# Optimization experiments

Measured on AMD Instinct MI355X. Metric: run time of the kernel, lower is better.

## Reference

```python
import jax, jax.numpy as jnp
import numpy as np

N = 8192
F_IN = 256
F_OUT = 64
ALPHA = 0.2  # LeakyReLU negative slope
NEG_INF = -9e15


def setup_inputs() -> dict:
    key = jax.random.key(0)
    k1, k2, k3, k4 = jax.random.split(key, 4)
    h = jax.random.normal(k1, (N, F_IN), dtype=jnp.float32)
    adj = jax.random.randint(k2, (N, N), 0, 2, dtype=jnp.int32)
    W = jax.random.normal(k3, (F_IN, F_OUT), dtype=jnp.float32) * 0.1
    a = jax.random.normal(k4, (2 * F_OUT, 1), dtype=jnp.float32) * 0.1
    return {"h": h, "adj": adj, "W": W, "a": a}


def reference(h, adj, W, a):
    # Wh: [N, F_out]
    Wh = h @ W
    # e_ij = LeakyReLU(a1 . Wh_i + a2 . Wh_j); same math as the O(N^2*2F)
    # concat in the original, computed via two [N] gathers + broadcast add.
    f_src = Wh @ a[:F_OUT, 0]   # [N] contribution of node i (row)
    f_dst = Wh @ a[F_OUT:, 0]   # [N] contribution of node j (col)
    e = f_src[:, None] + f_dst[None, :]          # [N, N]
    e = jnp.where(e > 0, e, ALPHA * e)           # LeakyReLU
    # masked softmax over neighbors (dim=1)
    e = jnp.where(adj > 0, e, NEG_INF)
    attention = jax.nn.softmax(e, axis=1)        # [N, N]
    h_prime = attention @ Wh                     # [N, F_out]
    # concat=True -> ELU
    return jax.nn.elu(h_prime)
```

## Files before the change

### kernel.cpp

```cpp
#include <hip/hip_runtime.h>
#include <math.h>

#define N 8192
#define FIN 256
#define FOUT 64
#define ALPHA 0.2f
#define LOG2E 1.442695040888963f

#define JT 256
#define NTILE (N / JT)
#define ROWPITCH 512
#define OFF_B 0
#define OFF_A (64 * ROWPITCH)
#define BUFB (OFF_A + 16 * ROWPITCH)
#define SMEM_BYTES (2 * BUFB)

typedef float f32x4 __attribute__((ext_vector_type(4)));
typedef _Float16 f16x8 __attribute__((ext_vector_type(8)));

__device__ __forceinline__ unsigned pack_f16(float a, float b) {
    union { _Float16 h; unsigned short u; } ca, cb;
    ca.h = (_Float16)a; cb.h = (_Float16)b;
    return (unsigned)ca.u | ((unsigned)cb.u << 16);
}
__device__ __forceinline__ float wcalc(int av, float fsr, float g) {
    float e = fsr + g;
    float le = e > 0.f ? e : ALPHA * e;
    float r = __builtin_exp2f(fmaf(le, LOG2E, -4.0f));
    return av != 0 ? r : 0.f;
}

__global__ __launch_bounds__(256) void gat_prep(
    const float* __restrict__ h, const float* __restrict__ W,
    const float* __restrict__ a,
    float* __restrict__ fsrc, float* __restrict__ fdst,
    unsigned short* __restrict__ WhT)
{
    __shared__ float sWh[16][FOUT + 1];
    const int t = threadIdx.x;
    const int f = t & 63;
    const int wq = t >> 6;
    const int row0 = blockIdx.x * 16;
    const int rbase = row0 + wq * 4;

    float acc[4] = {0.f, 0.f, 0.f, 0.f};
    for (int k0 = 0; k0 < FIN; k0 += 4) {
        const float w0 = W[(k0 + 0) * FOUT + f];
        const float w1 = W[(k0 + 1) * FOUT + f];
        const float w2 = W[(k0 + 2) * FOUT + f];
        const float w3 = W[(k0 + 3) * FOUT + f];
#pragma unroll
        for (int rr = 0; rr < 4; ++rr) {
            const float4 hv = *reinterpret_cast<const float4*>(
                &h[(size_t)(rbase + rr) * FIN + k0]);
            acc[rr] = fmaf(hv.x, w0, acc[rr]);
            acc[rr] = fmaf(hv.y, w1, acc[rr]);
            acc[rr] = fmaf(hv.z, w2, acc[rr]);
            acc[rr] = fmaf(hv.w, w3, acc[rr]);
        }
    }
    const float as = a[f], ad = a[FOUT + f];
#pragma unroll
    for (int rr = 0; rr < 4; ++rr) {
        sWh[wq * 4 + rr][f] = acc[rr];
        float fs = acc[rr] * as, fd = acc[rr] * ad;
#pragma unroll
        for (int off = 1; off < 64; off <<= 1) {
            fs += __shfl_xor(fs, off, 64);
            fd += __shfl_xor(fd, off, 64);
        }
        if (f == 0) { fsrc[rbase + rr] = fs; fdst[rbase + rr] = fd; }
    }
    __syncthreads();
    const int ff = t >> 2;
    const int r4 = (t & 3) * 4;
    uint2 v;
    v.x = pack_f16(sWh[r4 + 0][ff], sWh[r4 + 1][ff]);
    v.y = pack_f16(sWh[r4 + 2][ff], sWh[r4 + 3][ff]);
    *reinterpret_cast<uint2*>(&WhT[(size_t)ff * N + row0 + r4]) = v;
}

struct Regs { int4 a0, a1; float4 g0, g1; int4 b0, b1, b2, b3; };

__global__ __launch_bounds__(512, 4) void gat_main(
    const int* __restrict__ adj,
    const unsigned short* __restrict__ WhT,
    const float* __restrict__ fsrc, const float* __restrict__ fdst,
    float* __restrict__ out)
{
    __shared__ __align__(16) char smem[SMEM_BYTES];

    const int t = threadIdx.x;
    const int l = t & 63;
    const int w = t >> 6;
    const int row0 = blockIdx.x * 16;

    const int srow = t >> 5;
    const int sc8 = (t & 31) * 8;
    const int bf = t >> 3;
    const int bg = t & 7;
    const float fsr = fsrc[row0 + srow];
    const size_t adjrow = (size_t)(row0 + srow) * N;
    const size_t bfrow = (size_t)bf * N;

    const int aswz = (srow & 7) << 4;
    const int bswz = (bf & 7) << 4;
    const int awo  = OFF_A + srow * ROWPITCH + (((t & 31) * 16) ^ aswz);
    const int bwo0 = OFF_B + bf * ROWPITCH + (((bg + 0) * 16) ^ bswz);
    const int bwo1 = OFF_B + bf * ROWPITCH + (((bg + 8) * 16) ^ bswz);
    const int bwo2 = OFF_B + bf * ROWPITCH + (((bg + 16) * 16) ^ bswz);
    const int bwo3 = OFF_B + bf * ROWPITCH + (((bg + 24) * 16) ^ bswz);

    const int ft = w & 3;
    const int p = w >> 2;
    const int r16 = l & 15;
    const int kg8 = (l >> 4) << 3;
    const int fswz = (r16 & 7) << 4;
    const int aro = OFF_A + r16 * ROWPITCH;
    const int bro = OFF_B + (ft * 16 + r16) * ROWPITCH;

    f32x4 acc = {0.f, 0.f, 0.f, 0.f};
    float zacc = 0.f;
    Regs RA, RB;

#define BAR                                                                    \
    {                                                                          \
        asm volatile("s_waitcnt lgkmcnt(0)" ::: "memory");                     \
        __builtin_amdgcn_s_barrier();                                          \
    }

#define LOADG(tile, S)                                                         \
    {                                                                          \
        const int j0_ = (tile) * JT;                                           \
        S.a0 = *reinterpret_cast<const int4*>(&adj[adjrow + j0_ + sc8]);       \
        S.a1 = *reinterpret_cast<const int4*>(&adj[adjrow + j0_ + sc8 + 4]);   \
        S.g0 = *reinterpret_cast<const float4*>(&fdst[j0_ + sc8]);             \
        S.g1 = *reinterpret_cast<const float4*>(&fdst[j0_ + sc8 + 4]);         \
        S.b0 = *reinterpret_cast<const int4*>(&WhT[bfrow + j0_ + (bg+0)*8]);   \
        S.b1 = *reinterpret_cast<const int4*>(&WhT[bfrow + j0_ + (bg+8)*8]);   \
        S.b2 = *reinterpret_cast<const int4*>(&WhT[bfrow + j0_ + (bg+16)*8]);  \
        S.b3 = *reinterpret_cast<const int4*>(&WhT[bfrow + j0_ + (bg+24)*8]);  \
    }

#define STAGE(S, BUF)                                                          \
    {                                                                          \
        char* bs_ = smem + (BUF) * BUFB;                                       \
        *reinterpret_cast<int4*>(bs_ + bwo0) = S.b0;                           \
        *reinterpret_cast<int4*>(bs_ + bwo1) = S.b1;                           \
        *reinterpret_cast<int4*>(bs_ + bwo2) = S.b2;                           \
        *reinterpret_cast<int4*>(bs_ + bwo3) = S.b3;                           \
        const float w0 = wcalc(S.a0.x, fsr, S.g0.x);                           \
        const float w1 = wcalc(S.a0.y, fsr, S.g0.y);                           \
        const float w2 = wcalc(S.a0.z, fsr, S.g0.z);                           \
        const float w3 = wcalc(S.a0.w, fsr, S.g0.w);                           \
        const float w4 = wcalc(S.a1.x, fsr, S.g1.x);                           \
        const float w5 = wcalc(S.a1.y, fsr, S.g1.y);                           \
        const float w6 = wcalc(S.a1.z, fsr, S.g1.z);                           \
        const float w7 = wcalc(S.a1.w, fsr, S.g1.w);                           \
        zacc += (w0 + w1) + (w2 + w3) + ((w4 + w5) + (w6 + w7));               \
        uint4 pk;                                                              \
        pk.x = pack_f16(w0, w1); pk.y = pack_f16(w2, w3);                      \
        pk.z = pack_f16(w4, w5); pk.w = pack_f16(w6, w7);                      \
        *reinterpret_cast<uint4*>(bs_ + awo) = pk;                             \
    }

#define MFMA_PHASE(BUF)                                                        \
    {                                                                          \
        const char* bb_ = smem + (BUF) * BUFB;                                 \
        __builtin_amdgcn_s_setprio(1);                                         \
        _Pragma("unroll")                                                      \
        for (int ks = 0; ks < 4; ++ks) {                                       \
            const int cb = (p * 128 + ks * 32 + kg8) * 2;                      \
            const f16x8 af = *reinterpret_cast<const f16x8*>(bb_ + aro + (cb ^ fswz)); \
            const f16x8 bv = *reinterpret_cast<const f16x8*>(bb_ + bro + (cb ^ fswz)); \
            acc = __builtin_amdgcn_mfma_f32_16x16x32_f16(af, bv, acc, 0, 0, 0);\
        }                                                                      \
        __builtin_amdgcn_s_setprio(0);                                         \
    }

    LOADG(0, RA);
    LOADG(1, RB);
    STAGE(RA, 0);
    LOADG(2, RA);
    BAR;

    for (int tt = 0; tt < NTILE; tt += 2) {
        if (tt + 1 < NTILE) STAGE(RB, 1);
        if (tt + 3 < NTILE) LOADG(tt + 3, RB);
        MFMA_PHASE(0);
        BAR;
        if (tt + 2 < NTILE) STAGE(RA, 0);
        if (tt + 4 < NTILE) LOADG(tt + 4, RA);
        if (tt + 1 < NTILE) MFMA_PHASE(1);
        BAR;
    }
#undef LOADG
#undef STAGE
#undef MFMA_PHASE
#undef BAR

    float* zb = reinterpret_cast<float*>(smem + 8192);
    {
        float z = zacc;
#pragma unroll
        for (int off = 1; off < 32; off <<= 1) z += __shfl_xor(z, off, 64);
        if ((l & 31) == 0) zb[srow] = z;
    }

    *reinterpret_cast<f32x4*>(smem + w * 1024 + l * 16) = acc;
    __syncthreads();
#pragma unroll
    for (int e0 = 0; e0 < 2; ++e0) {
        const int e = t + e0 * 512;
        const int rr = e >> 6, f2 = e & 63;
        const int ft2 = f2 >> 4, n = f2 & 15;
        const int ln = n | ((rr >> 2) << 4);
        const int rg = rr & 3;
        const float s =
            *reinterpret_cast<const float*>(smem + ft2 * 1024 + ln * 16 + rg * 4) +
            *reinterpret_cast<const float*>(smem + (ft2 + 4) * 1024 + ln * 16 + rg * 4);
        const float hp = s / zb[rr];
        out[(size_t)(row0 + rr) * FOUT + f2] = hp > 0.f ? hp : expm1f(hp);
    }
}

extern "C" void kernel_launch(void* const* d_in, const int* in_sizes, int n_in,
                              void* d_out, int out_size, void* d_ws, size_t ws_size,
                              hipStream_t stream) {
    const float* h   = (const float*)d_in[0];
    const int*   adj = (const int*)d_in[1];
    const float* W   = (const float*)d_in[2];
    const float* a   = (const float*)d_in[3];
    float* out = (float*)d_out;

    float* ws = (float*)d_ws;
    float* fsrc = ws;
    float* fdst = fsrc + N;
    unsigned short* WhT = (unsigned short*)(fdst + N);

    gat_prep<<<dim3(N / 16), dim3(256), 0, stream>>>(h, W, a, fsrc, fdst, WhT);
    gat_main<<<dim3(N / 16), dim3(512), 0, stream>>>(adj, WhT, fsrc, fdst, out);
}
```

Baseline: 92.75 us.

## Prepack Wh into MFMA fragment layout and load B operands directly to registers

The prep kernel now writes Wh in a pre-swizzled MFMA B-fragment layout. The main kernel therefore loads B operands straight from global memory into registers and no longer stages them through LDS. This cuts LDS traffic and LDS footprint, which allows the launch-bounds occupancy hint to rise from 4 to 6. The pipeline is reordered to single-buffer the adj/fdst registers, and the prep kernel uses 32-row blocks. The cost is that each wave issues more redundant global/L2 reads of B, since these are no longer shared via LDS across the waves of a block.

```diff
diff --git a/kernel.cpp b/kernel.cpp
--- a/kernel.cpp
+++ b/kernel.cpp
@@ -10,13 +10,13 @@
 #define JT 256
 #define NTILE (N / JT)
 #define ROWPITCH 512
-#define OFF_B 0
-#define OFF_A (64 * ROWPITCH)
-#define BUFB (OFF_A + 16 * ROWPITCH)
-#define SMEM_BYTES (2 * BUFB)
+#define ABUF (16 * ROWPITCH)
+#define SMEM_BYTES (2 * ABUF)
 
 typedef float f32x4 __attribute__((ext_vector_type(4)));
 typedef _Float16 f16x8 __attribute__((ext_vector_type(8)));
+
+union F16V { uint4 u; f16x8 h; };
 
 __device__ __forceinline__ unsigned pack_f16(float a, float b) {
     union { _Float16 h; unsigned short u; } ca, cb;
@@ -30,17 +30,17 @@
     return av != 0 ? r : 0.f;
 }
 
-__global__ __launch_bounds__(256) void gat_prep(
+__global__ __launch_bounds__(512) void gat_prep(
     const float* __restrict__ h, const float* __restrict__ W,
     const float* __restrict__ a,
     float* __restrict__ fsrc, float* __restrict__ fdst,
-    unsigned short* __restrict__ WhT)
+    uint4* __restrict__ Bp)
 {
-    __shared__ float sWh[16][FOUT + 1];
+    __shared__ float sWh[32][FOUT + 1];
     const int t = threadIdx.x;
     const int f = t & 63;
     const int wq = t >> 6;
-    const int row0 = blockIdx.x * 16;
+    const int row0 = blockIdx.x * 32;
     const int rbase = row0 + wq * 4;
 
     float acc[4] = {0.f, 0.f, 0.f, 0.f};
@@ -72,19 +72,27 @@
         if (f == 0) { fsrc[rbase + rr] = fs; fdst[rbase + rr] = fd; }
     }
     __syncthreads();
-    const int ff = t >> 2;
-    const int r4 = (t & 3) * 4;
-    uint2 v;
-    v.x = pack_f16(sWh[r4 + 0][ff], sWh[r4 + 1][ff]);
-    v.y = pack_f16(sWh[r4 + 2][ff], sWh[r4 + 3][ff]);
-    *reinterpret_cast<uint2*>(&WhT[(size_t)ff * N + row0 + r4]) = v;
-}
-
-struct Regs { int4 a0, a1; float4 g0, g1; int4 b0, b1, b2, b3; };
-
-__global__ __launch_bounds__(512, 4) void gat_main(
+    if (t < 256) {
+        const int ft = t >> 6;
+        const int l = t & 63;
+        const int li = l & 15, g = l >> 4;
+        float v[8];
+#pragma unroll
+        for (int e = 0; e < 8; ++e) v[e] = sWh[g * 8 + e][ft * 16 + li];
+        uint4 pk;
+        pk.x = pack_f16(v[0], v[1]);
+        pk.y = pack_f16(v[2], v[3]);
+        pk.z = pack_f16(v[4], v[5]);
+        pk.w = pack_f16(v[6], v[7]);
+        Bp[(size_t)(blockIdx.x * 4 + ft) * 64 + l] = pk;
+    }
+}
+
+struct AdjG { int4 a0, a1; float4 g0, g1; };
+
+__global__ __launch_bounds__(512, 6) void gat_main(
     const int* __restrict__ adj,
-    const unsigned short* __restrict__ WhT,
+    const uint4* __restrict__ Bp,
     const float* __restrict__ fsrc, const float* __restrict__ fdst,
     float* __restrict__ out)
 {
@@ -97,31 +105,22 @@
 
     const int srow = t >> 5;
     const int sc8 = (t & 31) * 8;
-    const int bf = t >> 3;
-    const int bg = t & 7;
     const float fsr = fsrc[row0 + srow];
     const size_t adjrow = (size_t)(row0 + srow) * N;
-    const size_t bfrow = (size_t)bf * N;
-
-    const int aswz = (srow & 7) << 4;
-    const int bswz = (bf & 7) << 4;
-    const int awo  = OFF_A + srow * ROWPITCH + (((t & 31) * 16) ^ aswz);
-    const int bwo0 = OFF_B + bf * ROWPITCH + (((bg + 0) * 16) ^ bswz);
-    const int bwo1 = OFF_B + bf * ROWPITCH + (((bg + 8) * 16) ^ bswz);
-    const int bwo2 = OFF_B + bf * ROWPITCH + (((bg + 16) * 16) ^ bswz);
-    const int bwo3 = OFF_B + bf * ROWPITCH + (((bg + 24) * 16) ^ bswz);
+    const int awo = srow * ROWPITCH + (((t & 31) * 16) ^ ((srow & 7) << 4));
 
     const int ft = w & 3;
     const int p = w >> 2;
     const int r16 = l & 15;
     const int kg8 = (l >> 4) << 3;
     const int fswz = (r16 & 7) << 4;
-    const int aro = OFF_A + r16 * ROWPITCH;
-    const int bro = OFF_B + (ft * 16 + r16) * ROWPITCH;
+    const int aro = r16 * ROWPITCH;
+    const uint4* Bq = Bp + (size_t)p * 1024 + ft * 64 + l;
 
     f32x4 acc = {0.f, 0.f, 0.f, 0.f};
     float zacc = 0.f;
-    Regs RA, RB;
+    AdjG AG;
+    uint4 BA0, BA1, BA2, BA3, BB0, BB1, BB2, BB3;
 
 #define BAR                                                                    \
     {                                                                          \
@@ -129,76 +128,88 @@
         __builtin_amdgcn_s_barrier();                                          \
     }
 
-#define LOADG(tile, S)                                                         \
+#define LOAD_ADJG(tile)                                                        \
     {                                                                          \
         const int j0_ = (tile) * JT;                                           \
-        S.a0 = *reinterpret_cast<const int4*>(&adj[adjrow + j0_ + sc8]);       \
-        S.a1 = *reinterpret_cast<const int4*>(&adj[adjrow + j0_ + sc8 + 4]);   \
-        S.g0 = *reinterpret_cast<const float4*>(&fdst[j0_ + sc8]);             \
-        S.g1 = *reinterpret_cast<const float4*>(&fdst[j0_ + sc8 + 4]);         \
-        S.b0 = *reinterpret_cast<const int4*>(&WhT[bfrow + j0_ + (bg+0)*8]);   \
-        S.b1 = *reinterpret_cast<const int4*>(&WhT[bfrow + j0_ + (bg+8)*8]);   \
-        S.b2 = *reinterpret_cast<const int4*>(&WhT[bfrow + j0_ + (bg+16)*8]);  \
-        S.b3 = *reinterpret_cast<const int4*>(&WhT[bfrow + j0_ + (bg+24)*8]);  \
-    }
-
-#define STAGE(S, BUF)                                                          \
-    {                                                                          \
-        char* bs_ = smem + (BUF) * BUFB;                                       \
-        *reinterpret_cast<int4*>(bs_ + bwo0) = S.b0;                           \
-        *reinterpret_cast<int4*>(bs_ + bwo1) = S.b1;                           \
-        *reinterpret_cast<int4*>(bs_ + bwo2) = S.b2;                           \
-        *reinterpret_cast<int4*>(bs_ + bwo3) = S.b3;                           \
-        const float w0 = wcalc(S.a0.x, fsr, S.g0.x);                           \
-        const float w1 = wcalc(S.a0.y, fsr, S.g0.y);                           \
-        const float w2 = wcalc(S.a0.z, fsr, S.g0.z);                           \
-        const float w3 = wcalc(S.a0.w, fsr, S.g0.w);                           \
-        const float w4 = wcalc(S.a1.x, fsr, S.g1.x);                           \
-        const float w5 = wcalc(S.a1.y, fsr, S.g1.y);                           \
-        const float w6 = wcalc(S.a1.z, fsr, S.g1.z);                           \
-        const float w7 = wcalc(S.a1.w, fsr, S.g1.w);                           \
+        AG.a0 = *reinterpret_cast<const int4*>(&adj[adjrow + j0_ + sc8]);      \
+        AG.a1 = *reinterpret_cast<const int4*>(&adj[adjrow + j0_ + sc8 + 4]);  \
+        AG.g0 = *reinterpret_cast<const float4*>(&fdst[j0_ + sc8]);            \
+        AG.g1 = *reinterpret_cast<const float4*>(&fdst[j0_ + sc8 + 4]);        \
+    }
+
+#define LOAD_B(tile, B0, B1, B2, B3)                                           \
+    {                                                                          \
+        const uint4* bq_ = Bq + (size_t)(tile) * 2048;                         \
+        B0 = bq_[0];                                                           \
+        B1 = bq_[256];                                                         \
+        B2 = bq_[512];                                                         \
+        B3 = bq_[768];                                                         \
+    }
+
+#define STAGE(BUF)                                                             \
+    {                                                                          \
+        const float w0 = wcalc(AG.a0.x, fsr, AG.g0.x);                         \
+        const float w1 = wcalc(AG.a0.y, fsr, AG.g0.y);                         \
+        const float w2 = wcalc(AG.a0.z, fsr, AG.g0.z);                         \
+        const float w3 = wcalc(AG.a0.w, fsr, AG.g0.w);                         \
+        const float w4 = wcalc(AG.a1.x, fsr, AG.g1.x);                         \
+        const float w5 = wcalc(AG.a1.y, fsr, AG.g1.y);                         \
+        const float w6 = wcalc(AG.a1.z, fsr, AG.g1.z);                         \
+        const float w7 = wcalc(AG.a1.w, fsr, AG.g1.w);                         \
         zacc += (w0 + w1) + (w2 + w3) + ((w4 + w5) + (w6 + w7));               \
         uint4 pk;                                                              \
         pk.x = pack_f16(w0, w1); pk.y = pack_f16(w2, w3);                      \
         pk.z = pack_f16(w4, w5); pk.w = pack_f16(w6, w7);                      \
-        *reinterpret_cast<uint4*>(bs_ + awo) = pk;                             \
-    }
-
-#define MFMA_PHASE(BUF)                                                        \
-    {                                                                          \
-        const char* bb_ = smem + (BUF) * BUFB;                                 \
+        *reinterpret_cast<uint4*>(smem + (BUF) * ABUF + awo) = pk;             \
+    }
+
+#define MFMA_PHASE(BUF, B0, B1, B2, B3)                                        \
+    {                                                                          \
+        const char* ab_ = smem + (BUF) * ABUF + aro;                           \
+        F16V a0v, a1v, a2v, a3v, b0v, b1v, b2v, b3v;                           \
+        a0v.u = *reinterpret_cast<const uint4*>(ab_ + (((p * 128 + 0 * 32 + kg8) * 2) ^ fswz)); \
+        a1v.u = *reinterpret_cast<const uint4*>(ab_ + (((p * 128 + 1 * 32 + kg8) * 2) ^ fswz)); \
+        a2v.u = *reinterpret_cast<const uint4*>(ab_ + (((p * 128 + 2 * 32 + kg8) * 2) ^ fswz)); \
+        a3v.u = *reinterpret_cast<const uint4*>(ab_ + (((p * 128 + 3 * 32 + kg8) * 2) ^ fswz)); \
+        b0v.u = B0; b1v.u = B1; b2v.u = B2; b3v.u = B3;                        \
         __builtin_amdgcn_s_setprio(1);                                         \
-        _Pragma("unroll")                                                      \
-        for (int ks = 0; ks < 4; ++ks) {                                       \
-            const int cb = (p * 128 + ks * 32 + kg8) * 2;                      \
-            const f16x8 af = *reinterpret_cast<const f16x8*>(bb_ + aro + (cb ^ fswz)); \
-            const f16x8 bv = *reinterpret_cast<const f16x8*>(bb_ + bro + (cb ^ fswz)); \
-            acc = __builtin_amdgcn_mfma_f32_16x16x32_f16(af, bv, acc, 0, 0, 0);\
-        }                                                                      \
+        acc = __builtin_amdgcn_mfma_f32_16x16x32_f16(a0v.h, b0v.h, acc, 0, 0, 0); \
+        acc = __builtin_amdgcn_mfma_f32_16x16x32_f16(a1v.h, b1v.h, acc, 0, 0, 0); \
+        acc = __builtin_amdgcn_mfma_f32_16x16x32_f16(a2v.h, b2v.h, acc, 0, 0, 0); \
+        acc = __builtin_amdgcn_mfma_f32_16x16x32_f16(a3v.h, b3v.h, acc, 0, 0, 0); \
         __builtin_amdgcn_s_setprio(0);                                         \
     }
 
-    LOADG(0, RA);
-    LOADG(1, RB);
-    STAGE(RA, 0);
-    LOADG(2, RA);
+    LOAD_ADJG(0);
+    LOAD_B(0, BA0, BA1, BA2, BA3);
+    STAGE(0);
+    LOAD_ADJG(1);
     BAR;
 
     for (int tt = 0; tt < NTILE; tt += 2) {
-        if (tt + 1 < NTILE) STAGE(RB, 1);
-        if (tt + 3 < NTILE) LOADG(tt + 3, RB);
-        MFMA_PHASE(0);
+        if (tt + 1 < NTILE) LOAD_B(tt + 1, BB0, BB1, BB2, BB3);
+        MFMA_PHASE(0, BA0, BA1, BA2, BA3);
+        {
+            STAGE(1);
+            if (tt + 2 < NTILE) LOAD_ADJG(tt + 2);
+        }
         BAR;
-        if (tt + 2 < NTILE) STAGE(RA, 0);
-        if (tt + 4 < NTILE) LOADG(tt + 4, RA);
-        if (tt + 1 < NTILE) MFMA_PHASE(1);
+        if (tt + 2 < NTILE) LOAD_B(tt + 2, BA0, BA1, BA2, BA3);
+        MFMA_PHASE(1, BB0, BB1, BB2, BB3);
+        if (tt + 2 < NTILE) {
+            STAGE(0);
+            if (tt + 3 < NTILE) LOAD_ADJG(tt + 3);
+        }
         BAR;
     }
-#undef LOADG
+#undef LOAD_ADJG
+#undef LOAD_B
 #undef STAGE
 #undef MFMA_PHASE
 #undef BAR
 
+    __syncthreads();
+
     float* zb = reinterpret_cast<float*>(smem + 8192);
     {
         float z = zacc;
@@ -206,7 +217,6 @@
         for (int off = 1; off < 32; off <<= 1) z += __shfl_xor(z, off, 64);
         if ((l & 31) == 0) zb[srow] = z;
     }
-
     *reinterpret_cast<f32x4*>(smem + w * 1024 + l * 16) = acc;
     __syncthreads();
 #pragma unroll
@@ -236,8 +246,8 @@
     float* ws = (float*)d_ws;
     float* fsrc = ws;
     float* fdst = fsrc + N;
-    unsigned short* WhT = (unsigned short*)(fdst + N);
-
-    gat_prep<<<dim3(N / 16), dim3(256), 0, stream>>>(h, W, a, fsrc, fdst, WhT);
-    gat_main<<<dim3(N / 16), dim3(512), 0, stream>>>(adj, WhT, fsrc, fdst, out);
-}
+    uint4* Bp = (uint4*)(fdst + N);
+
+    gat_prep<<<dim3(N / 32), dim3(512), 0, stream>>>(h, W, a, fsrc, fdst, Bp);
+    gat_main<<<dim3(N / 16), dim3(512), 0, stream>>>(adj, Bp, fsrc, fdst, out);
+}
```

After: 123.6 us. +33.3%, slower.
